# Performance work log

Hardware: AMD Instinct MI355X
Metric: run time of the kernel (lower is better)

Reference implementation:

```python
import jax, jax.numpy as jnp
import numpy as np

# sorted irreps after merging time embedding: 144x0e + 128x1o
S = 144   # scalar (0e) multiplicity: 16 (time embedding) + 128 (node feature scalars)
V = 128   # vector (1o) multiplicity
FS = 128  # scalar part of node features
INV_SQRT3 = 1.0 / np.sqrt(3.0)  # component-normalized CG for 1o x 1o -> 0e (dot/sqrt(3))


def setup_inputs() -> dict:
    key = jax.random.key(0)
    ks = jax.random.split(key, 9)
    N = 4096
    return {
        "flat_node_features": jax.random.normal(ks[0], (N, FS + 3 * V), jnp.float32),
        "flat_times": jax.random.uniform(ks[1], (N, 1), jnp.float32),
        # time embedding o3.Linear 1x0e -> 16x0e
        "W_t": jax.random.normal(ks[2], (1, 16), jnp.float32),
        # linear_1: per-l block linear on 144x0e + 128x1o
        "W1_s": jax.random.normal(ks[3], (S, S), jnp.float32),
        "W1_v": jax.random.normal(ks[4], (V, V), jnp.float32),
        # TensorSquare path weights: strict-upper triangle = 'u<v' paths, diagonal = 'uuw' paths
        "Wss": jax.random.normal(ks[5], (S, S, S), jnp.float32),  # 0e x 0e -> 0e
        "Wsv": jax.random.normal(ks[6], (S, V, V), jnp.float32),  # 0e x 1o -> 1o ('uvw')
        "Wvv": jax.random.normal(ks[7], (V, V, S), jnp.float32),  # 1o x 1o -> 0e
        # linear_2: 128x1o -> 1x1o
        "W2": jax.random.normal(ks[8], (V, 1), jnp.float32),
    }


def _forward(feat, times, W_t, W1_s, W1_v, Wss, Wsv, Wvv, W2):
    N = feat.shape[0]
    # time embedding (fan_in = 1) + concat + (identity) permutation into sorted irreps
    emb = times @ W_t                                   # [N,16]
    s = jnp.concatenate([emb, feat[:, :FS]], axis=1)    # [N,S] scalars (0e)
    v = feat[:, FS:].reshape(N, V, 3)                   # [N,V,3] vectors (1o)

    # linear_1 (irreps-wise, fan_in normalized)
    s1 = (s @ W1_s) / np.sqrt(S)                        # [N,S]
    v1 = jnp.einsum("num,uw->nwm", v, W1_v) / np.sqrt(V)  # [N,V,3]

    # ---- TensorSquare (sorted -> sorted) ----
    mask_s = jnp.triu(jnp.ones((S, S), s1.dtype), 1)
    mask_v = jnp.triu(jnp.ones((V, V), v1.dtype), 1)

    # path A: 0e x 0e -> 0e, 'u<v'
    WssU = Wss * mask_s[:, :, None]
    tA = jnp.einsum("nvw,nv->nw", jnp.einsum("nu,uvw->nvw", s1, WssU), s1)
    tA = tA / np.sqrt(S * (S - 1) / 2)
    # path B: 0e x 0e -> 0e, 'uuw' (diagonal u==v)
    tB = jnp.einsum("nu,uw->nw", s1 * s1, jnp.einsum("uuw->uw", Wss)) / np.sqrt(S)
    # path C: 1o x 1o -> 0e, 'u<v'  (CG = dot/sqrt(3))
    D = jnp.einsum("num,nvm->nuv", v1, v1) * INV_SQRT3   # [N,V,V]
    tC = jnp.einsum("nuv,uvw->nw", D, Wvv * mask_v[:, :, None]) / np.sqrt(V * (V - 1) / 2)
    # path D: 1o x 1o -> 0e, 'uuw'
    norms = jnp.sum(v1 * v1, axis=-1) * INV_SQRT3        # [N,V]
    tD = jnp.einsum("nu,uw->nw", norms, jnp.einsum("uuw->uw", Wvv)) / np.sqrt(V)
    s2 = (tA + tB + tC + tD) / np.sqrt(4.0)              # 4 paths into 0e

    # path E: 0e x 1o -> 1o, 'uvw' (single path; CG identity under component norm)
    tmp = jnp.einsum("nu,uvw->nvw", s1, Wsv) / np.sqrt(S * V)  # [N,V,V]
    v2 = jnp.einsum("nvw,nvm->nwm", tmp, v1)             # [N,V,3]

    # gated nonlinearity: silu on scalar (l=0) channel only
    s3 = jax.nn.silu(s2)
    del s3  # scalars do not feed linear_2 (irreps_out = 1x1o has no 0e path)

    # linear_2: 128x1o -> 1x1o
    out = jnp.einsum("num,uk->nkm", v2, W2)[:, 0, :] / np.sqrt(V)  # [N,3]
    return out


def reference(flat_node_features, flat_times, W_t, W1_s, W1_v, Wss, Wsv, Wvv, W2):
    return _forward(flat_node_features, flat_times, W_t, W1_s, W1_v, Wss, Wsv, Wvv, W2)
```

## Files before the change

### kernel.cpp

```cpp
#include <hip/hip_runtime.h>
#include <hip/hip_bf16.h>
#include <math.h>


#define S 144
#define V 128

typedef __attribute__((ext_vector_type(8))) short bf16x8;
typedef __attribute__((ext_vector_type(4))) float f32x4;

__global__ __launch_bounds__(256) void kE(const float* __restrict__ Wsv,
                                          const float* __restrict__ W2,
                                          const float* __restrict__ W1v,
                                          unsigned short* __restrict__ Et) {
    __shared__ float Dsh[V];
    __shared__ float Epart[2][V];
    const int tid = threadIdx.x;
    const int wave = tid >> 6;
    const int lane = tid & 63;
    const int half = lane >> 5;
    const int j = lane & 31;
    const int u = blockIdx.x;

    const float4* Wsv4 = (const float4*)Wsv;
    const float4 w4 = ((const float4*)W2)[j];
    const size_t base4 = ((size_t)u * V + 32 * wave) * 32;
    float4 a[16];
#pragma unroll
    for (int i = 0; i < 16; ++i)
        a[i] = Wsv4[base4 + (size_t)(2 * i + half) * 32 + j];
#pragma unroll
    for (int i = 0; i < 16; ++i) {
        float acc = a[i].x * w4.x + a[i].y * w4.y + a[i].z * w4.z + a[i].w * w4.w;
#pragma unroll
        for (int off = 1; off < 32; off <<= 1)
            acc += __shfl_xor(acc, off, 64);
        if (j == 0) Dsh[32 * wave + 2 * i + half] = acc;
    }
    __syncthreads();

    const int c = tid & 127, vh = tid >> 7;
    const float4* W1v4 = (const float4*)W1v;
    const float4* D4 = (const float4*)Dsh;
    float acc = 0.f;
#pragma unroll
    for (int i = 0; i < 16; ++i) {
        const float4 wv = W1v4[c * 32 + vh * 16 + i];
        const float4 dv = D4[vh * 16 + i];
        acc += wv.x * dv.x + wv.y * dv.y + wv.z * dv.z + wv.w * dv.w;
    }
    Epart[vh][c] = acc;
    __syncthreads();
    if (tid < V) {
        const float scale = 1.0f / (144.0f * 128.0f * sqrtf(128.0f));
        const float val = scale * (Epart[0][tid] + Epart[1][tid]);
        const __hip_bfloat16 hb = __float2bfloat16(val);
        Et[(size_t)tid * S + u] = *(const unsigned short*)&hb;
    }
}

__global__ __launch_bounds__(256) void k4b(const float* __restrict__ feat,
                                           const float* __restrict__ times,
                                           const float* __restrict__ Wt,
                                           const float* __restrict__ W1s,
                                           const unsigned short* __restrict__ EtG,
                                           float* __restrict__ out) {
    __shared__ unsigned short Ash[144][168];
    __shared__ unsigned short Etsh[128][168];
    __shared__ unsigned short Mtsh[128][136];
    __shared__ unsigned short srow[16][136];
    __shared__ float bsh[128];
    __shared__ float tsh[16];
    __shared__ float red[4][16][3];
    const int tid = threadIdx.x;
    const int wave = tid >> 6;
    const int lane = tid & 63;
    const int n0 = blockIdx.x * 16;
    const int mrow = lane & 15;
    const int kch = lane >> 4;

#pragma unroll
    for (int i = 0; i < 18; ++i) {
        const int idx = tid + 256 * i;
        const int row = idx / 36;
        const int c4 = (idx % 36) * 4;
        const float4 f = *(const float4*)(W1s + (size_t)(16 + row) * S + c4);
        const __hip_bfloat162 p0 = __float22bfloat162_rn(make_float2(f.x, f.y));
        const __hip_bfloat162 p1 = __float22bfloat162_rn(make_float2(f.z, f.w));
        uint2 pk;
        pk.x = *(const unsigned*)&p0;
        pk.y = *(const unsigned*)&p1;
        *(uint2*)&Ash[row][c4] = pk;
    }
    if (tid < S) {
        float a = 0.f;
#pragma unroll
        for (int p = 0; p < 16; ++p)
            a = fmaf(Wt[p], W1s[p * S + tid], a);
        const __hip_bfloat16 hb = __float2bfloat16(a);
        Ash[128][tid] = *(const unsigned short*)&hb;
    }
    for (int i = tid; i < 864; i += 256) {
        const int row = i / 6, c4 = 144 + (i % 6) * 4;
        *(unsigned long long*)&Ash[row][c4] = 0ULL;
    }
    for (int i = tid; i < 768; i += 256) {
        const int row = i / 6, c4 = 144 + (i % 6) * 4;
        *(unsigned long long*)&Etsh[row][c4] = 0ULL;
    }
    {
        const uint4 z4 = {0u, 0u, 0u, 0u};
        for (int i = tid; i < 315; i += 256) {
            const int row = 129 + i / 21;
            const int c8 = (i % 21) * 8;
            *(uint4*)&Ash[row][c8] = z4;
        }
    }
    {
        const uint4* src = (const uint4*)EtG;
#pragma unroll
        for (int i = 0; i < 9; ++i) {
            const int idx = tid + 256 * i;
            const int row = idx / 18;
            const int c8 = (idx % 18) * 8;
            *(uint4*)&Etsh[row][c8] = src[idx];
        }
    }
    {
        const int r = tid >> 4, q0 = (tid & 15) * 8;
        const float* p = feat + (size_t)(n0 + r) * 512 + q0;
        const float4 f0 = *(const float4*)(p);
        const float4 f1 = *(const float4*)(p + 4);
        const __hip_bfloat162 p0 = __float22bfloat162_rn(make_float2(f0.x, f0.y));
        const __hip_bfloat162 p1 = __float22bfloat162_rn(make_float2(f0.z, f0.w));
        const __hip_bfloat162 p2 = __float22bfloat162_rn(make_float2(f1.x, f1.y));
        const __hip_bfloat162 p3 = __float22bfloat162_rn(make_float2(f1.z, f1.w));
        uint4 pk;
        pk.x = *(const unsigned*)&p0;
        pk.y = *(const unsigned*)&p1;
        pk.z = *(const unsigned*)&p2;
        pk.w = *(const unsigned*)&p3;
        *(uint4*)&srow[r][q0] = pk;
    }
    if (tid < 16) tsh[tid] = times[n0 + tid];
    __syncthreads();

    bf16x8 Bf[2][5];
#pragma unroll
    for (int c2 = 0; c2 < 2; ++c2)
#pragma unroll
        for (int kk = 0; kk < 5; ++kk)
            Bf[c2][kk] = *(const bf16x8*)&Etsh[(2 * wave + c2) * 16 + mrow][kk * 32 + kch * 8];

#pragma unroll
    for (int rt = 0; rt < 9; ++rt) {
        bf16x8 Af[5];
#pragma unroll
        for (int kk = 0; kk < 5; ++kk)
            Af[kk] = *(const bf16x8*)&Ash[rt * 16 + mrow][kk * 32 + kch * 8];
#pragma unroll
        for (int c2 = 0; c2 < 2; ++c2) {
            f32x4 acc = {0.f, 0.f, 0.f, 0.f};
#pragma unroll
            for (int kk = 0; kk < 5; ++kk)
                acc = __builtin_amdgcn_mfma_f32_16x16x32_bf16(Af[kk], Bf[c2][kk], acc, 0, 0, 0);
            const int c = (2 * wave + c2) * 16 + mrow;
            if (rt < 8) {
#pragma unroll
                for (int i = 0; i < 4; ++i) {
                    const int q = rt * 16 + kch * 4 + i;
                    const __hip_bfloat16 hb = __float2bfloat16(acc[i]);
                    Mtsh[c][q] = *(const unsigned short*)&hb;
                }
            } else if (kch == 0) {
                bsh[c] = acc[0];
            }
        }
    }
    __syncthreads();

    const float bc0 = bsh[32 * wave + mrow];
    const float bc1 = bsh[32 * wave + 16 + mrow];
    f32x4 acc0 = {0.f, 0.f, 0.f, 0.f};
    f32x4 acc1 = {0.f, 0.f, 0.f, 0.f};
#pragma unroll
    for (int kk = 0; kk < 4; ++kk) {
        const bf16x8 af = *(const bf16x8*)&srow[mrow][kk * 32 + kch * 8];
        const bf16x8 bf0 = *(const bf16x8*)&Mtsh[32 * wave + mrow][kk * 32 + kch * 8];
        const bf16x8 bf1 = *(const bf16x8*)&Mtsh[32 * wave + 16 + mrow][kk * 32 + kch * 8];
        acc0 = __builtin_amdgcn_mfma_f32_16x16x32_bf16(af, bf0, acc0, 0, 0, 0);
        acc1 = __builtin_amdgcn_mfma_f32_16x16x32_bf16(af, bf1, acc1, 0, 0, 0);
    }

    float pm[4][3];
#pragma unroll
    for (int i = 0; i < 4; ++i) {
        const int nr = kch * 4 + i;
        const float t = tsh[nr];
        const float h0 = acc0[i] + t * bc0;
        const float h1 = acc1[i] + t * bc1;
        const float* vp0 = feat + (size_t)(n0 + nr) * 512 + V + 3 * (32 * wave + mrow);
        const float* vp1 = vp0 + 48;
#pragma unroll
        for (int m = 0; m < 3; ++m)
            pm[i][m] = vp0[m] * h0 + vp1[m] * h1;
    }
#pragma unroll
    for (int i = 0; i < 4; ++i) {
#pragma unroll
        for (int m = 0; m < 3; ++m) {
            float v = pm[i][m];
            v += __shfl_xor(v, 1, 64);
            v += __shfl_xor(v, 2, 64);
            v += __shfl_xor(v, 4, 64);
            v += __shfl_xor(v, 8, 64);
            pm[i][m] = v;
        }
        if (mrow == 0) {
            const int nr = kch * 4 + i;
            red[wave][nr][0] = pm[i][0];
            red[wave][nr][1] = pm[i][1];
            red[wave][nr][2] = pm[i][2];
        }
    }
    __syncthreads();
    if (tid < 48) {
        const int nr = tid / 3, m = tid % 3;
        out[(size_t)(n0 + nr) * 3 + m] =
            red[0][nr][m] + red[1][nr][m] + red[2][nr][m] + red[3][nr][m];
    }
}

extern "C" void kernel_launch(void* const* d_in, const int* in_sizes, int n_in,
                              void* d_out, int out_size, void* d_ws, size_t ws_size,
                              hipStream_t stream) {
    const float* feat  = (const float*)d_in[0];
    const float* times = (const float*)d_in[1];
    const float* Wt    = (const float*)d_in[2];
    const float* W1s   = (const float*)d_in[3];
    const float* W1v   = (const float*)d_in[4];
    const float* Wsv   = (const float*)d_in[6];
    const float* W2    = (const float*)d_in[8];

    unsigned short* Et = (unsigned short*)d_ws;

    kE<<<dim3(144), dim3(256), 0, stream>>>(Wsv, W2, W1v, Et);
    k4b<<<dim3(256), dim3(256), 0, stream>>>(feat, times, Wt, W1s, Et, (float*)d_out);
}
```

Before: 17.77 us.

## Reassociate per-block matmul chain to compute s1 first instead of W1s·E product

Each block used to form the 144x128 product of W1s and E (M = W1s·E) and then multiply its 16 node rows by M. It now computes z = s·W1s plus the time-bias term for its 16 rows first, then multiplies z by E. This cuts per-block MFMA work from about 9x8 tiles down to roughly 9 plus 8 tile sets. Shared memory use also shrinks because one buffer is reused for the transposed W1s and then E, at the cost of an extra barrier and transposing scalar stores into LDS.

```diff
diff --git a/kernel.cpp b/kernel.cpp
--- a/kernel.cpp
+++ b/kernel.cpp
@@ -8,6 +8,11 @@
 
 typedef __attribute__((ext_vector_type(8))) short bf16x8;
 typedef __attribute__((ext_vector_type(4))) float f32x4;
+
+__device__ inline unsigned short f2bf(float x) {
+    const __hip_bfloat16 h = __float2bfloat16(x);
+    return *(const unsigned short*)&h;
+}
 
 __global__ __launch_bounds__(256) void kE(const float* __restrict__ Wsv,
                                           const float* __restrict__ W2,
@@ -53,23 +58,20 @@
     __syncthreads();
     if (tid < V) {
         const float scale = 1.0f / (144.0f * 128.0f * sqrtf(128.0f));
-        const float val = scale * (Epart[0][tid] + Epart[1][tid]);
-        const __hip_bfloat16 hb = __float2bfloat16(val);
-        Et[(size_t)tid * S + u] = *(const unsigned short*)&hb;
-    }
-}
-
-__global__ __launch_bounds__(256) void k4b(const float* __restrict__ feat,
+        Et[(size_t)tid * S + u] = f2bf(scale * (Epart[0][tid] + Epart[1][tid]));
+    }
+}
+
+__global__ __launch_bounds__(256) void k4c(const float* __restrict__ feat,
                                            const float* __restrict__ times,
                                            const float* __restrict__ Wt,
                                            const float* __restrict__ W1s,
                                            const unsigned short* __restrict__ EtG,
                                            float* __restrict__ out) {
-    __shared__ unsigned short Ash[144][168];
-    __shared__ unsigned short Etsh[128][168];
-    __shared__ unsigned short Mtsh[128][136];
+    __shared__ unsigned short Bsh[21504];
     __shared__ unsigned short srow[16][136];
-    __shared__ float bsh[128];
+    __shared__ unsigned short zsh[16][168];
+    __shared__ float wtld[S];
     __shared__ float tsh[16];
     __shared__ float red[4][16][3];
     const int tid = threadIdx.x;
@@ -79,52 +81,12 @@
     const int mrow = lane & 15;
     const int kch = lane >> 4;
 
-#pragma unroll
-    for (int i = 0; i < 18; ++i) {
-        const int idx = tid + 256 * i;
-        const int row = idx / 36;
-        const int c4 = (idx % 36) * 4;
-        const float4 f = *(const float4*)(W1s + (size_t)(16 + row) * S + c4);
-        const __hip_bfloat162 p0 = __float22bfloat162_rn(make_float2(f.x, f.y));
-        const __hip_bfloat162 p1 = __float22bfloat162_rn(make_float2(f.z, f.w));
-        uint2 pk;
-        pk.x = *(const unsigned*)&p0;
-        pk.y = *(const unsigned*)&p1;
-        *(uint2*)&Ash[row][c4] = pk;
-    }
-    if (tid < S) {
-        float a = 0.f;
-#pragma unroll
-        for (int p = 0; p < 16; ++p)
-            a = fmaf(Wt[p], W1s[p * S + tid], a);
-        const __hip_bfloat16 hb = __float2bfloat16(a);
-        Ash[128][tid] = *(const unsigned short*)&hb;
-    }
-    for (int i = tid; i < 864; i += 256) {
-        const int row = i / 6, c4 = 144 + (i % 6) * 4;
-        *(unsigned long long*)&Ash[row][c4] = 0ULL;
-    }
-    for (int i = tid; i < 768; i += 256) {
-        const int row = i / 6, c4 = 144 + (i % 6) * 4;
-        *(unsigned long long*)&Etsh[row][c4] = 0ULL;
-    }
-    {
-        const uint4 z4 = {0u, 0u, 0u, 0u};
-        for (int i = tid; i < 315; i += 256) {
-            const int row = 129 + i / 21;
-            const int c8 = (i % 21) * 8;
-            *(uint4*)&Ash[row][c8] = z4;
-        }
-    }
-    {
-        const uint4* src = (const uint4*)EtG;
-#pragma unroll
-        for (int i = 0; i < 9; ++i) {
-            const int idx = tid + 256 * i;
-            const int row = idx / 18;
-            const int c8 = (idx % 18) * 8;
-            *(uint4*)&Etsh[row][c8] = src[idx];
-        }
+    uint4 etr[9];
+    {
+        const uint4* esrc = (const uint4*)EtG;
+#pragma unroll
+        for (int i = 0; i < 9; ++i)
+            etr[i] = esrc[tid + 256 * i];
     }
     {
         const int r = tid >> 4, q0 = (tid & 15) * 8;
@@ -140,54 +102,80 @@
         pk.y = *(const unsigned*)&p1;
         pk.z = *(const unsigned*)&p2;
         pk.w = *(const unsigned*)&p3;
-        *(uint4*)&srow[r][q0] = pk;
+        *(uint4*)&srow[tid >> 4][q0] = pk;
+    }
+#pragma unroll
+    for (int i = 0; i < 18; ++i) {
+        const int idx = tid + 256 * i;
+        const int q = idx / 36;
+        const int u0 = (idx % 36) * 4;
+        const float4 f = *(const float4*)(W1s + (size_t)(16 + q) * S + u0);
+        Bsh[(u0 + 0) * 136 + q] = f2bf(f.x);
+        Bsh[(u0 + 1) * 136 + q] = f2bf(f.y);
+        Bsh[(u0 + 2) * 136 + q] = f2bf(f.z);
+        Bsh[(u0 + 3) * 136 + q] = f2bf(f.w);
+    }
+    if (tid < S) {
+        float a = 0.f;
+#pragma unroll
+        for (int p = 0; p < 16; ++p)
+            a = fmaf(Wt[p], W1s[p * S + tid], a);
+        wtld[tid] = a;
+    }
+    if (tid < 64) {
+        const int row = tid >> 2, c4 = 144 + (tid & 3) * 4;
+        *(unsigned long long*)&zsh[row][c4] = 0ULL;
     }
     if (tid < 16) tsh[tid] = times[n0 + tid];
     __syncthreads();
 
-    bf16x8 Bf[2][5];
-#pragma unroll
-    for (int c2 = 0; c2 < 2; ++c2)
-#pragma unroll
-        for (int kk = 0; kk < 5; ++kk)
-            Bf[c2][kk] = *(const bf16x8*)&Etsh[(2 * wave + c2) * 16 + mrow][kk * 32 + kch * 8];
-
-#pragma unroll
-    for (int rt = 0; rt < 9; ++rt) {
-        bf16x8 Af[5];
-#pragma unroll
-        for (int kk = 0; kk < 5; ++kk)
-            Af[kk] = *(const bf16x8*)&Ash[rt * 16 + mrow][kk * 32 + kch * 8];
-#pragma unroll
-        for (int c2 = 0; c2 < 2; ++c2) {
+    {
+        bf16x8 Af[4];
+#pragma unroll
+        for (int kk = 0; kk < 4; ++kk)
+            Af[kk] = *(const bf16x8*)&srow[mrow][kk * 32 + kch * 8];
+        const int tstart = (wave == 0) ? 0 : (wave * 2 + 1);
+        const int tcnt = (wave == 0) ? 3 : 2;
+        for (int tt = 0; tt < tcnt; ++tt) {
+            const int ti = tstart + tt;
             f32x4 acc = {0.f, 0.f, 0.f, 0.f};
 #pragma unroll
-            for (int kk = 0; kk < 5; ++kk)
-                acc = __builtin_amdgcn_mfma_f32_16x16x32_bf16(Af[kk], Bf[c2][kk], acc, 0, 0, 0);
-            const int c = (2 * wave + c2) * 16 + mrow;
-            if (rt < 8) {
-#pragma unroll
-                for (int i = 0; i < 4; ++i) {
-                    const int q = rt * 16 + kch * 4 + i;
-                    const __hip_bfloat16 hb = __float2bfloat16(acc[i]);
-                    Mtsh[c][q] = *(const unsigned short*)&hb;
-                }
-            } else if (kch == 0) {
-                bsh[c] = acc[0];
+            for (int kk = 0; kk < 4; ++kk) {
+                const bf16x8 bf = *(const bf16x8*)&Bsh[(ti * 16 + mrow) * 136 + kk * 32 + kch * 8];
+                acc = __builtin_amdgcn_mfma_f32_16x16x32_bf16(Af[kk], bf, acc, 0, 0, 0);
+            }
+            const int u = ti * 16 + mrow;
+            const float wu = wtld[u];
+#pragma unroll
+            for (int i = 0; i < 4; ++i) {
+                const int n = kch * 4 + i;
+                zsh[n][u] = f2bf(acc[i] + tsh[n] * wu);
             }
         }
     }
     __syncthreads();
 
-    const float bc0 = bsh[32 * wave + mrow];
-    const float bc1 = bsh[32 * wave + 16 + mrow];
+#pragma unroll
+    for (int i = 0; i < 9; ++i) {
+        const int idx = tid + 256 * i;
+        const int c = idx / 18;
+        const int u8 = (idx % 18) * 8;
+        *(uint4*)&Bsh[c * 168 + u8] = etr[i];
+    }
+    {
+        const uint4 z4 = {0u, 0u, 0u, 0u};
+        const int c = tid >> 1, u8 = 144 + (tid & 1) * 8;
+        *(uint4*)&Bsh[c * 168 + u8] = z4;
+    }
+    __syncthreads();
+
     f32x4 acc0 = {0.f, 0.f, 0.f, 0.f};
     f32x4 acc1 = {0.f, 0.f, 0.f, 0.f};
 #pragma unroll
-    for (int kk = 0; kk < 4; ++kk) {
-        const bf16x8 af = *(const bf16x8*)&srow[mrow][kk * 32 + kch * 8];
-        const bf16x8 bf0 = *(const bf16x8*)&Mtsh[32 * wave + mrow][kk * 32 + kch * 8];
-        const bf16x8 bf1 = *(const bf16x8*)&Mtsh[32 * wave + 16 + mrow][kk * 32 + kch * 8];
+    for (int kk = 0; kk < 5; ++kk) {
+        const bf16x8 af = *(const bf16x8*)&zsh[mrow][kk * 32 + kch * 8];
+        const bf16x8 bf0 = *(const bf16x8*)&Bsh[(32 * wave + mrow) * 168 + kk * 32 + kch * 8];
+        const bf16x8 bf1 = *(const bf16x8*)&Bsh[(32 * wave + 16 + mrow) * 168 + kk * 32 + kch * 8];
         acc0 = __builtin_amdgcn_mfma_f32_16x16x32_bf16(af, bf0, acc0, 0, 0, 0);
         acc1 = __builtin_amdgcn_mfma_f32_16x16x32_bf16(af, bf1, acc1, 0, 0, 0);
     }
@@ -196,9 +184,8 @@
 #pragma unroll
     for (int i = 0; i < 4; ++i) {
         const int nr = kch * 4 + i;
-        const float t = tsh[nr];
-        const float h0 = acc0[i] + t * bc0;
-        const float h1 = acc1[i] + t * bc1;
+        const float h0 = acc0[i];
+        const float h1 = acc1[i];
         const float* vp0 = feat + (size_t)(n0 + nr) * 512 + V + 3 * (32 * wave + mrow);
         const float* vp1 = vp0 + 48;
 #pragma unroll
@@ -245,5 +232,5 @@
     unsigned short* Et = (unsigned short*)d_ws;
 
     kE<<<dim3(144), dim3(256), 0, stream>>>(Wsv, W2, W1v, Et);
-    k4b<<<dim3(256), dim3(256), 0, stream>>>(feat, times, Wt, W1s, Et, (float*)d_out);
-}
+    k4c<<<dim3(256), dim3(256), 0, stream>>>(feat, times, Wt, W1s, Et, (float*)d_out);
+}
```

Result: slower. 22.46 us (+26.4%).
